# Optimization experiments

Measured on AMD Instinct MI355X. Metric: run time of the kernel, lower is better.

Reference implementation:

```python
import jax, jax.numpy as jnp
import numpy as np

N = 50000
E = 800000
IN_CH = 256
OUT_CH = 64   # per-head channels (PyG out_channels)
HEADS = 4
NEG_SLOPE = 0.2


def setup_inputs() -> dict:
    key = jax.random.key(0)
    k = jax.random.split(key, 8)
    x = jax.random.normal(k[0], (N, IN_CH), dtype=jnp.float32)
    edge_index = jax.random.randint(k[1], (2, E), 0, N, dtype=jnp.int64)
    # GATConv parameters
    W = jax.random.normal(k[2], (IN_CH, HEADS * OUT_CH), dtype=jnp.float32) * (1.0 / np.sqrt(IN_CH))
    att_src = jax.random.normal(k[3], (HEADS, OUT_CH), dtype=jnp.float32) * 0.1
    att_dst = jax.random.normal(k[4], (HEADS, OUT_CH), dtype=jnp.float32) * 0.1
    bias = jnp.zeros((OUT_CH,), dtype=jnp.float32)
    # residual linear (bias=False)
    W_res = jax.random.normal(k[5], (IN_CH, OUT_CH), dtype=jnp.float32) * (1.0 / np.sqrt(IN_CH))
    return {"x": x, "edge_index": edge_index, "W": W, "att_src": att_src,
            "att_dst": att_dst, "bias": bias, "W_res": W_res}


def _gat_forward(x, edge_index, W, att_src, att_dst, bias, W_res):
    # residual branch
    x_res = x @ W_res                                   # [N, OUT_CH]

    # node transform: [N, H, C]
    xw = (x @ W).reshape(N, HEADS, OUT_CH)
    # per-node attention logits, [N, H]
    a_src = jnp.einsum('nhc,hc->nh', xw, att_src)
    a_dst = jnp.einsum('nhc,hc->nh', xw, att_dst)

    # add self-loops (PyG GATConv default add_self_loops=True)
    loops = jnp.arange(N, dtype=edge_index.dtype)
    src = jnp.concatenate([edge_index[0], loops])       # [E+N]
    dst = jnp.concatenate([edge_index[1], loops])       # [E+N]

    # per-edge logits + leaky relu, [E+N, H]
    alpha = jax.nn.leaky_relu(a_src[src] + a_dst[dst], NEG_SLOPE)

    # segment softmax over destination nodes
    m = jax.ops.segment_max(alpha, dst, num_segments=N)    # [N, H]
    e = jnp.exp(alpha - m[dst])
    denom = jax.ops.segment_sum(e, dst, num_segments=N)    # [N, H]
    a = e / denom[dst]                                     # [E+N, H]
    # (dropout p=0.1 on attention coeffs is identity in eval mode)

    # weighted scatter-aggregate: [N, H, C]
    msgs = xw[src] * a[:, :, None]
    out = jax.ops.segment_sum(msgs, dst, num_segments=N)

    # concat=False -> mean over heads, then bias
    x_conv = out.mean(axis=1) + bias                     # [N, OUT_CH]
    return jax.nn.relu(x_conv + x_res)


def reference(x, edge_index, W, att_src, att_dst, bias, W_res):
    return _gat_forward(x, edge_index, W, att_src, att_dst, bias, W_res)
```

## Files before the change

kernel.cpp:

```cpp
#include <hip/hip_runtime.h>
#include <math.h>

#define N_NODES 50000
#define N_EDGES 800000
#define IN_CH   256
#define OUT_CH  64
#define HEADS   4
#define NEG_SLOPE 0.2f
#define NCOLS   320
#define NTILES  20
#define NKK     8
#define PACK_BLOCKS 40
#define GEMM_BLOCKS 782
#define NBINS   391
#define P1_BLOCKS 256
#define EPB     3125
#define AGG_BLOCKS 6250
#define STASH_CAP 2816

typedef __attribute__((ext_vector_type(8))) short short8;
typedef __attribute__((ext_vector_type(4))) float f32x4;

__device__ __forceinline__ float lrelu(float v) {
    return v > 0.f ? v : NEG_SLOPE * v;
}
__device__ __forceinline__ unsigned bf16_rne(float f) {
    unsigned u = __float_as_uint(f);
    return (u + 0x7FFFu + ((u >> 16) & 1u)) >> 16;
}
__device__ __forceinline__ unsigned pack2(float lo, float hi) {
    return bf16_rne(lo) | (bf16_rne(hi) << 16);
}
__device__ __forceinline__ float bflo(unsigned u) { return __uint_as_float(u << 16); }
__device__ __forceinline__ float bfhi(unsigned u) { return __uint_as_float(u & 0xFFFF0000u); }
__device__ __forceinline__ short8 as_short8(uint4 u) {
    union { uint4 u4; short8 s8; } cv; cv.u4 = u; return cv.s8;
}

__global__ __launch_bounds__(256) void pack_B(
    const float* __restrict__ W, const float* __restrict__ Wres,
    uint4* __restrict__ Bp)
{
    const int idx  = blockIdx.x * 256 + threadIdx.x;
    const int kk   = idx / (NTILES * 64);
    const int rem  = idx - kk * (NTILES * 64);
    const int t    = rem >> 6;
    const int lane = rem & 63;
    const int colL = lane & 15, quad = lane >> 4;
    const int col  = t * 16 + colL;
    const int k0   = kk * 32 + quad * 8;
    float v[8];
    #pragma unroll
    for (int j = 0; j < 8; ++j) {
        const int k = k0 + j;
        v[j] = (col < IN_CH) ? W[(size_t)k * IN_CH + col]
                             : Wres[(size_t)k * OUT_CH + (col - IN_CH)];
    }
    uint4 u;
    u.x = pack2(v[0], v[1]); u.y = pack2(v[2], v[3]);
    u.z = pack2(v[4], v[5]); u.w = pack2(v[6], v[7]);
    Bp[(kk * NTILES + t) * 64 + lane] = u;
}

__global__ __launch_bounds__(256) void gemm_hist(
    const float* __restrict__ x, const uint4* __restrict__ Bp,
    uint2* __restrict__ xw2, float* __restrict__ xres,
    const int* __restrict__ ei, int* __restrict__ M,
    const float* __restrict__ attS, const float* __restrict__ attD,
    float* __restrict__ asrc, float* __restrict__ adst)
{
    __shared__ uint4 Alds[4 * NKK * 64];
    __shared__ float logS[64][HEADS];
    __shared__ float logD[64][HEADS];

    if (blockIdx.x >= GEMM_BLOCKS) {
        const int blk = blockIdx.x - GEMM_BLOCKS;
        int* lh = (int*)Alds;
        for (int b = threadIdx.x; b < NBINS; b += 256) lh[b] = 0;
        __syncthreads();
        const int e0 = blk * EPB;
        #pragma unroll
        for (int r = 0; r < 13; ++r) {
            const int idx = (r << 8) + threadIdx.x;
            if (idx < EPB)
                atomicAdd(&lh[ei[N_EDGES + e0 + idx] >> 7], 1);
        }
        __syncthreads();
        for (int b = threadIdx.x; b < NBINS; b += 256)
            M[(size_t)b * P1_BLOCKS + blk] = lh[b];
        return;
    }

    const int tid = threadIdx.x;
    const int n0  = blockIdx.x * 64;

    logS[tid >> 2][tid & 3] = 0.f;
    logD[tid >> 2][tid & 3] = 0.f;

    #pragma unroll
    for (int i = 0; i < 8; ++i) {
        const int e    = i * 256 + tid;
        const int g    = e >> 9;
        const int kk   = (e >> 6) & 7;
        const int lane = e & 63;
        const int cL   = lane & 15, qd = lane >> 4;
        const int row  = n0 + g * 16 + cL;
        const int k0   = kk * 32 + qd * 8;
        uint4 u = make_uint4(0u, 0u, 0u, 0u);
        if (row < N_NODES) {
            const float4 a = *reinterpret_cast<const float4*>(x + (size_t)row * IN_CH + k0);
            const float4 b = *reinterpret_cast<const float4*>(x + (size_t)row * IN_CH + k0 + 4);
            u.x = pack2(a.x, a.y); u.y = pack2(a.z, a.w);
            u.z = pack2(b.x, b.y); u.w = pack2(b.z, b.w);
        }
        Alds[(g * NKK + kk) * 64 + lane] = u;
    }
    __syncthreads();

    const int lane = tid & 63;
    const int wv   = tid >> 6;
    const int colL = lane & 15, quad = lane >> 4;

    f32x4 acc[4][5];
    #pragma unroll
    for (int rg = 0; rg < 4; ++rg)
        #pragma unroll
        for (int j = 0; j < 5; ++j) acc[rg][j] = (f32x4){0.f, 0.f, 0.f, 0.f};

    for (int kk = 0; kk < NKK; ++kk) {
        uint4 bu[5];
        #pragma unroll
        for (int j = 0; j < 5; ++j)
            bu[j] = Bp[(kk * NTILES + j * 4 + wv) * 64 + lane];
        #pragma unroll
        for (int rg = 0; rg < 4; ++rg) {
            const short8 a = as_short8(Alds[(rg * NKK + kk) * 64 + lane]);
            #pragma unroll
            for (int j = 0; j < 5; ++j)
                acc[rg][j] = __builtin_amdgcn_mfma_f32_16x16x32_bf16(
                    a, as_short8(bu[j]), acc[rg][j], 0, 0, 0);
        }
    }

    #pragma unroll
    for (int rg = 0; rg < 4; ++rg) {
        #pragma unroll
        for (int r = 0; r < 4; ++r) {
            const int row = n0 + rg * 16 + quad * 4 + r;
            if (row < N_NODES) {
                xw2[(size_t)row * 64 + wv * 16 + colL] = make_uint2(
                    pack2(acc[rg][0][r], acc[rg][1][r]),
                    pack2(acc[rg][2][r], acc[rg][3][r]));
                xres[(size_t)row * OUT_CH + wv * 16 + colL] = acc[rg][4][r];
            }
        }
    }

    float aSr[HEADS], aDr[HEADS];
    #pragma unroll
    for (int h = 0; h < HEADS; ++h) {
        aSr[h] = attS[h * 64 + wv * 16 + colL];
        aDr[h] = attD[h * 64 + wv * 16 + colL];
    }
    #pragma unroll
    for (int rg = 0; rg < 4; ++rg) {
        #pragma unroll
        for (int h = 0; h < HEADS; ++h) {
            #pragma unroll
            for (int r = 0; r < 4; ++r) {
                float vS = acc[rg][h][r] * aSr[h];
                float vD = acc[rg][h][r] * aDr[h];
                #pragma unroll
                for (int m = 1; m < 16; m <<= 1) {
                    vS += __shfl_xor(vS, m);
                    vD += __shfl_xor(vD, m);
                }
                if (colL == 0) {
                    atomicAdd(&logS[rg * 16 + quad * 4 + r][h], vS);
                    atomicAdd(&logD[rg * 16 + quad * 4 + r][h], vD);
                }
            }
        }
    }
    __syncthreads();
    {
        const int rl = tid >> 2, h = tid & 3;
        const int row = n0 + rl;
        if (row < N_NODES) {
            asrc[(size_t)row * HEADS + h] = logS[rl][h];
            adst[(size_t)row * HEADS + h] = logD[rl][h];
        }
    }
}

__global__ __launch_bounds__(256) void binscan_M(
    int* __restrict__ M, int* __restrict__ binCnt)
{
    __shared__ int ws[4];
    const int t = threadIdx.x, lane = t & 63, w = t >> 6;
    const int b = blockIdx.x;
    const int v = M[(size_t)b * P1_BLOCKS + t];
    int sc = v;
    #pragma unroll
    for (int off = 1; off < 64; off <<= 1) {
        const int n = __shfl_up(sc, off);
        if (lane >= off) sc += n;
    }
    if (lane == 63) ws[w] = sc;
    __syncthreads();
    int prefix = 0;
    for (int j = 0; j < w; ++j) prefix += ws[j];
    M[(size_t)b * P1_BLOCKS + t] = prefix + sc - v;
    if (t == 255) binCnt[b] = prefix + sc;
}

__global__ __launch_bounds__(256) void part_mid(
    const int* __restrict__ ei, const int* __restrict__ M,
    const int* __restrict__ binCnt, unsigned* __restrict__ mid)
{
    __shared__ int bc[NBINS];
    __shared__ int bs[NBINS];
    __shared__ int baseL[NBINS];
    __shared__ int lh[NBINS];
    __shared__ int ws[4];
    const int t = threadIdx.x, lane = t & 63, wv = t >> 6;
    const int blk = blockIdx.x;

    for (int b = t; b < NBINS; b += 256) {
        bc[b] = binCnt[b];
        baseL[b] = M[(size_t)b * P1_BLOCKS + blk];
        lh[b] = 0;
    }
    __syncthreads();

    int tot0;
    {
        const int v = bc[t];
        int sc = v;
        #pragma unroll
        for (int off = 1; off < 64; off <<= 1) {
            const int n = __shfl_up(sc, off);
            if (lane >= off) sc += n;
        }
        if (lane == 63) ws[wv] = sc;
        __syncthreads();
        int prefix = 0;
        for (int j = 0; j < wv; ++j) prefix += ws[j];
        bs[t] = prefix + sc - v;
        tot0 = ws[0] + ws[1] + ws[2] + ws[3];
        __syncthreads();
    }
    {
        const int i2 = 256 + t;
        const int v = (i2 < NBINS) ? bc[i2] : 0;
        int sc = v;
        #pragma unroll
        for (int off = 1; off < 64; off <<= 1) {
            const int n = __shfl_up(sc, off);
            if (lane >= off) sc += n;
        }
        if (lane == 63) ws[wv] = sc;
        __syncthreads();
        int prefix = 0;
        for (int j = 0; j < wv; ++j) prefix += ws[j];
        if (i2 < NBINS) bs[i2] = tot0 + prefix + sc - v;
        __syncthreads();
    }
    for (int b = t; b < NBINS; b += 256) baseL[b] += bs[b];
    __syncthreads();

    const int e0 = blk * EPB;
    #pragma unroll
    for (int r = 0; r < 13; ++r) {
        const int idx = (r << 8) + t;
        if (idx < EPB) {
            const int e = e0 + idx;
            const int d = ei[N_EDGES + e];
            const int b = d >> 7;
            const int pos = atomicAdd(&lh[b], 1);
            mid[baseL[b] + pos] = ((unsigned)(d & 127) << 17) | (unsigned)ei[e];
        }
    }
}

__global__ __launch_bounds__(256) void scatter_fine2(
    const unsigned* __restrict__ mid, const int* __restrict__ binCnt,
    int* __restrict__ cnt, int* __restrict__ lscan, int* __restrict__ esrc)
{
    __shared__ int ws[4];
    __shared__ int c128[128];
    __shared__ int o128[128];
    __shared__ int w0tot;
    __shared__ unsigned stash[STASH_CAP];
    const int t = threadIdx.x, lane = t & 63, wv = t >> 6;
    const int b = blockIdx.x;

    int acc = 0;
    for (int j = t; j < NBINS; j += 256)
        if (j < b) acc += binCnt[j];
    #pragma unroll
    for (int off = 32; off >= 1; off >>= 1) acc += __shfl_xor(acc, off);
    if (lane == 0) ws[wv] = acc;
    if (t < 128) c128[t] = 0;
    __syncthreads();
    const int base = ws[0] + ws[1] + ws[2] + ws[3];
    const int n = binCnt[b];

    for (int i = t; i < n; i += 256) {
        const unsigned m = mid[base + i];
        if (i < STASH_CAP) stash[i] = m;
        atomicAdd(&c128[m >> 17], 1);
    }
    __syncthreads();

    if (t < 128) {
        const int v = c128[t];
        int sc = v;
        #pragma unroll
        for (int off = 1; off < 64; off <<= 1) {
            const int nn = __shfl_up(sc, off);
            if (lane >= off) sc += nn;
        }
        if (t == 63) w0tot = sc;
        __syncthreads();
        const int ex = sc - v + (t >= 64 ? w0tot : 0);
        o128[t] = ex;
        const int d = (b << 7) + t;
        if (d < N_NODES) {
            cnt[d] = v;
            lscan[d] = base + ex;
        }
        c128[t] = 0;
    } else {
        __syncthreads();
    }
    __syncthreads();

    for (int i = t; i < n; i += 256) {
        const unsigned m = (i < STASH_CAP) ? stash[i] : mid[base + i];
        const int dlo = (int)(m >> 17);
        const int pos = atomicAdd(&c128[dlo], 1);
        esrc[base + o128[dlo] + pos] = (int)(m & 0x1FFFFu);
    }
}

__global__ __launch_bounds__(256) void aggregate(
    const int* __restrict__ esrc, const int* __restrict__ lscan,
    const int* __restrict__ cnt,
    const float* __restrict__ asrc, const float* __restrict__ adst,
    const uint2* __restrict__ xw2, const float* __restrict__ xres,
    const float* __restrict__ bias, float* __restrict__ out,
    const int d0)
{
    __shared__ float4 wbuf[4][64];
    __shared__ int    sbuf[4][64];
    const int t = threadIdx.x;
    const int lane = t & 63;
    const int wv   = t >> 6;

    const int d = d0 + blockIdx.x * 4 + wv;
    const int row = lscan[d];
    const int deg = cnt[d];
    const float4 ad = *reinterpret_cast<const float4*>(adst + (size_t)d * 4);
    const char* xwB = (const char*)xw2;
    const int laneB = lane << 3;

    float dn0 = 0.f, dn1 = 0.f, dn2 = 0.f, dn3 = 0.f;
    float ac0 = 0.f, ac1 = 0.f, ac2 = 0.f, ac3 = 0.f;

    for (int base = 0; base < deg; base += 64) {
        const int m = min(64, deg - base);
        if (lane < m) {
            const int s = esrc[row + base + lane];
            const float4 as = *reinterpret_cast<const float4*>(asrc + (size_t)s * 4);
            const float e0 = __expf(lrelu(as.x + ad.x));
            const float e1 = __expf(lrelu(as.y + ad.y));
            const float e2 = __expf(lrelu(as.z + ad.z));
            const float e3 = __expf(lrelu(as.w + ad.w));
            dn0 += e0; dn1 += e1; dn2 += e2; dn3 += e3;
            wbuf[wv][lane] = make_float4(e0, e1, e2, e3);
            sbuf[wv][lane] = s << 9;
        }
        int j = 0;
        for (; j + 4 <= m; j += 4) {
            uint2 v0 = *(const uint2*)(xwB + sbuf[wv][j]     + laneB);
            uint2 v1 = *(const uint2*)(xwB + sbuf[wv][j + 1] + laneB);
            uint2 v2 = *(const uint2*)(xwB + sbuf[wv][j + 2] + laneB);
            uint2 v3 = *(const uint2*)(xwB + sbuf[wv][j + 3] + laneB);
            {
                const float4 w = wbuf[wv][j];
                ac0 = fmaf(w.x, bflo(v0.x), ac0); ac1 = fmaf(w.y, bfhi(v0.x), ac1);
                ac2 = fmaf(w.z, bflo(v0.y), ac2); ac3 = fmaf(w.w, bfhi(v0.y), ac3);
            }
            {
                const float4 w = wbuf[wv][j + 1];
                ac0 = fmaf(w.x, bflo(v1.x), ac0); ac1 = fmaf(w.y, bfhi(v1.x), ac1);
                ac2 = fmaf(w.z, bflo(v1.y), ac2); ac3 = fmaf(w.w, bfhi(v1.y), ac3);
            }
            {
                const float4 w = wbuf[wv][j + 2];
                ac0 = fmaf(w.x, bflo(v2.x), ac0); ac1 = fmaf(w.y, bfhi(v2.x), ac1);
                ac2 = fmaf(w.z, bflo(v2.y), ac2); ac3 = fmaf(w.w, bfhi(v2.y), ac3);
            }
            {
                const float4 w = wbuf[wv][j + 3];
                ac0 = fmaf(w.x, bflo(v3.x), ac0); ac1 = fmaf(w.y, bfhi(v3.x), ac1);
                ac2 = fmaf(w.z, bflo(v3.y), ac2); ac3 = fmaf(w.w, bfhi(v3.y), ac3);
            }
        }
        for (; j < m; ++j) {
            const float4 w = wbuf[wv][j];
            const uint2 v = *(const uint2*)(xwB + sbuf[wv][j] + laneB);
            ac0 = fmaf(w.x, bflo(v.x), ac0);
            ac1 = fmaf(w.y, bfhi(v.x), ac1);
            ac2 = fmaf(w.z, bflo(v.y), ac2);
            ac3 = fmaf(w.w, bfhi(v.y), ac3);
        }
    }

    #pragma unroll
    for (int off = 32; off >= 1; off >>= 1) {
        dn0 += __shfl_xor(dn0, off);
        dn1 += __shfl_xor(dn1, off);
        dn2 += __shfl_xor(dn2, off);
        dn3 += __shfl_xor(dn3, off);
    }
    const float4 asd = *reinterpret_cast<const float4*>(asrc + (size_t)d * 4);
    const float s0 = __expf(lrelu(asd.x + ad.x));
    const float s1 = __expf(lrelu(asd.y + ad.y));
    const float s2 = __expf(lrelu(asd.z + ad.z));
    const float s3 = __expf(lrelu(asd.w + ad.w));
    const uint2 u = xw2[(size_t)d * 64 + lane];
    ac0 = fmaf(s0, bflo(u.x), ac0); ac1 = fmaf(s1, bfhi(u.x), ac1);
    ac2 = fmaf(s2, bflo(u.y), ac2); ac3 = fmaf(s3, bfhi(u.y), ac3);
    const float i0 = 0.25f / (dn0 + s0);
    const float i1 = 0.25f / (dn1 + s1);
    const float i2 = 0.25f / (dn2 + s2);
    const float i3 = 0.25f / (dn3 + s3);
    const float v = ac0 * i0 + ac1 * i1 + ac2 * i2 + ac3 * i3
                  + bias[lane] + xres[(size_t)d * OUT_CH + lane];
    out[(size_t)d * OUT_CH + lane] = fmaxf(v, 0.f);
}

extern "C" void kernel_launch(void* const* d_in, const int* in_sizes, int n_in,
                              void* d_out, int out_size, void* d_ws, size_t ws_size,
                              hipStream_t stream) {
    const float* x    = (const float*)d_in[0];
    const int*   ei   = (const int*)d_in[1];
    const float* W    = (const float*)d_in[2];
    const float* attS = (const float*)d_in[3];
    const float* attD = (const float*)d_in[4];
    const float* bias = (const float*)d_in[5];
    const float* Wres = (const float*)d_in[6];
    float* out = (float*)d_out;

    char* p = (char*)d_ws;
    uint4*    Bp      = (uint4*)p;    p += (size_t)NKK * NTILES * 64 * 16;
    uint2*    xw2     = (uint2*)p;    p += (size_t)N_NODES * 64 * 8;
    float*    xres    = (float*)p;    p += (size_t)N_NODES * OUT_CH * 4;
    float*    asrc    = (float*)p;    p += (size_t)N_NODES * HEADS * 4;
    float*    adst    = (float*)p;    p += (size_t)N_NODES * HEADS * 4;
    int*      M       = (int*)p;      p += (size_t)NBINS * P1_BLOCKS * 4;
    int*      binCnt  = (int*)p;      p += 512 * 4;
    int*      cnt     = (int*)p;      p += (size_t)N_NODES * 4;
    int*      lscan   = (int*)p;      p += (size_t)N_NODES * 4;
    unsigned* mid     = (unsigned*)p; p += (size_t)N_EDGES * 4;
    int*      esrc    = (int*)p;      p += (size_t)N_EDGES * 4;

    pack_B<<<PACK_BLOCKS, 256, 0, stream>>>(W, Wres, Bp);
    gemm_hist<<<GEMM_BLOCKS + P1_BLOCKS, 256, 0, stream>>>(
        x, Bp, xw2, xres, ei, M, attS, attD, asrc, adst);
    binscan_M<<<NBINS, 256, 0, stream>>>(M, binCnt);
    part_mid<<<P1_BLOCKS, 256, 0, stream>>>(ei, M, binCnt, mid);
    scatter_fine2<<<NBINS, 256, 0, stream>>>(mid, binCnt, cnt, lscan, esrc);
    aggregate<<<AGG_BLOCKS, 256, 0, stream>>>(
        esrc, lscan, cnt, asrc, adst, xw2, xres, bias, out, 0);
    aggregate<<<AGG_BLOCKS, 256, 0, stream>>>(
        esrc, lscan, cnt, asrc, adst, xw2, xres, bias, out, 25000);
}
```

Baseline: 237.5 us.

## Halve partition bin width, precompute bin starts, and merge aggregate launches

The counting-sort bins shrink from 128 to 64 destination nodes, doubling the bin count. That gives the fine scatter kernel twice as many smaller blocks and lets it drop to a single-wave 64-entry scan. Bin start offsets are now written once by part_mid instead of every scatter block re-summing all previous bin counts. The two half-range aggregate launches are merged into one launch, removing a kernel boundary. The cost is a larger histogram matrix M and a smaller LDS stash, so more large bins fall back to re-reading from global memory.

```diff
diff --git a/kernel.cpp b/kernel.cpp
--- a/kernel.cpp
+++ b/kernel.cpp
@@ -12,11 +12,11 @@
 #define NKK     8
 #define PACK_BLOCKS 40
 #define GEMM_BLOCKS 782
-#define NBINS   391
+#define NBINS   782
 #define P1_BLOCKS 256
 #define EPB     3125
-#define AGG_BLOCKS 6250
-#define STASH_CAP 2816
+#define AGG_BLOCKS 12500
+#define STASH_CAP 1280
 
 typedef __attribute__((ext_vector_type(8))) short short8;
 typedef __attribute__((ext_vector_type(4))) float f32x4;
@@ -83,7 +83,7 @@
         for (int r = 0; r < 13; ++r) {
             const int idx = (r << 8) + threadIdx.x;
             if (idx < EPB)
-                atomicAdd(&lh[ei[N_EDGES + e0 + idx] >> 7], 1);
+                atomicAdd(&lh[ei[N_EDGES + e0 + idx] >> 6], 1);
         }
         __syncthreads();
         for (int b = threadIdx.x; b < NBINS; b += 256)
@@ -216,7 +216,8 @@
 
 __global__ __launch_bounds__(256) void part_mid(
     const int* __restrict__ ei, const int* __restrict__ M,
-    const int* __restrict__ binCnt, unsigned* __restrict__ mid)
+    const int* __restrict__ binCnt, int* __restrict__ binStart,
+    unsigned* __restrict__ mid)
 {
     __shared__ int bc[NBINS];
     __shared__ int bs[NBINS];
@@ -233,40 +234,27 @@
     }
     __syncthreads();
 
-    int tot0;
-    {
-        const int v = bc[t];
+    int carry = 0;
+    for (int c = 0; c < 4; ++c) {
+        const int i = (c << 8) + t;
+        const int v = (i < NBINS) ? bc[i] : 0;
         int sc = v;
         #pragma unroll
-        for (int off = 1; off < 64; off <<= 1) {
-            const int n = __shfl_up(sc, off);
-            if (lane >= off) sc += n;
+        for (int o = 1; o < 64; o <<= 1) {
+            const int n = __shfl_up(sc, o);
+            if (lane >= o) sc += n;
         }
         if (lane == 63) ws[wv] = sc;
         __syncthreads();
         int prefix = 0;
         for (int j = 0; j < wv; ++j) prefix += ws[j];
-        bs[t] = prefix + sc - v;
-        tot0 = ws[0] + ws[1] + ws[2] + ws[3];
+        if (i < NBINS) bs[i] = carry + prefix + sc - v;
+        carry += ws[0] + ws[1] + ws[2] + ws[3];
         __syncthreads();
     }
-    {
-        const int i2 = 256 + t;
-        const int v = (i2 < NBINS) ? bc[i2] : 0;
-        int sc = v;
-        #pragma unroll
-        for (int off = 1; off < 64; off <<= 1) {
-            const int n = __shfl_up(sc, off);
-            if (lane >= off) sc += n;
-        }
-        if (lane == 63) ws[wv] = sc;
-        __syncthreads();
-        int prefix = 0;
-        for (int j = 0; j < wv; ++j) prefix += ws[j];
-        if (i2 < NBINS) bs[i2] = tot0 + prefix + sc - v;
-        __syncthreads();
-    }
     for (int b = t; b < NBINS; b += 256) baseL[b] += bs[b];
+    if (blk == 0)
+        for (int b = t; b < NBINS; b += 256) binStart[b] = bs[b];
     __syncthreads();
 
     const int e0 = blk * EPB;
@@ -276,71 +264,60 @@
         if (idx < EPB) {
             const int e = e0 + idx;
             const int d = ei[N_EDGES + e];
-            const int b = d >> 7;
+            const int b = d >> 6;
             const int pos = atomicAdd(&lh[b], 1);
-            mid[baseL[b] + pos] = ((unsigned)(d & 127) << 17) | (unsigned)ei[e];
+            mid[baseL[b] + pos] = ((unsigned)(d & 63) << 17) | (unsigned)ei[e];
         }
     }
 }
 
 __global__ __launch_bounds__(256) void scatter_fine2(
-    const unsigned* __restrict__ mid, const int* __restrict__ binCnt,
+    const unsigned* __restrict__ mid, const int* __restrict__ binStart,
+    const int* __restrict__ binCnt,
     int* __restrict__ cnt, int* __restrict__ lscan, int* __restrict__ esrc)
 {
-    __shared__ int ws[4];
-    __shared__ int c128[128];
-    __shared__ int o128[128];
-    __shared__ int w0tot;
+    __shared__ int c64[64];
+    __shared__ int o64[64];
     __shared__ unsigned stash[STASH_CAP];
-    const int t = threadIdx.x, lane = t & 63, wv = t >> 6;
+    const int t = threadIdx.x;
     const int b = blockIdx.x;
 
-    int acc = 0;
-    for (int j = t; j < NBINS; j += 256)
-        if (j < b) acc += binCnt[j];
-    #pragma unroll
-    for (int off = 32; off >= 1; off >>= 1) acc += __shfl_xor(acc, off);
-    if (lane == 0) ws[wv] = acc;
-    if (t < 128) c128[t] = 0;
-    __syncthreads();
-    const int base = ws[0] + ws[1] + ws[2] + ws[3];
+    const int base = binStart[b];
     const int n = binCnt[b];
+    if (t < 64) c64[t] = 0;
+    __syncthreads();
 
     for (int i = t; i < n; i += 256) {
         const unsigned m = mid[base + i];
         if (i < STASH_CAP) stash[i] = m;
-        atomicAdd(&c128[m >> 17], 1);
-    }
-    __syncthreads();
-
-    if (t < 128) {
-        const int v = c128[t];
+        atomicAdd(&c64[m >> 17], 1);
+    }
+    __syncthreads();
+
+    if (t < 64) {
+        const int v = c64[t];
         int sc = v;
         #pragma unroll
-        for (int off = 1; off < 64; off <<= 1) {
-            const int nn = __shfl_up(sc, off);
-            if (lane >= off) sc += nn;
-        }
-        if (t == 63) w0tot = sc;
-        __syncthreads();
-        const int ex = sc - v + (t >= 64 ? w0tot : 0);
-        o128[t] = ex;
-        const int d = (b << 7) + t;
+        for (int o = 1; o < 64; o <<= 1) {
+            const int nn = __shfl_up(sc, o);
+            if (t >= o) sc += nn;
+        }
+        const int ex = sc - v;
+        o64[t] = ex;
+        const int d = (b << 6) + t;
         if (d < N_NODES) {
             cnt[d] = v;
             lscan[d] = base + ex;
         }
-        c128[t] = 0;
-    } else {
-        __syncthreads();
+        c64[t] = 0;
     }
     __syncthreads();
 
     for (int i = t; i < n; i += 256) {
         const unsigned m = (i < STASH_CAP) ? stash[i] : mid[base + i];
         const int dlo = (int)(m >> 17);
-        const int pos = atomicAdd(&c128[dlo], 1);
-        esrc[base + o128[dlo] + pos] = (int)(m & 0x1FFFFu);
+        const int pos = atomicAdd(&c64[dlo], 1);
+        esrc[base + o64[dlo] + pos] = (int)(m & 0x1FFFFu);
     }
 }
 
@@ -349,8 +326,7 @@
     const int* __restrict__ cnt,
     const float* __restrict__ asrc, const float* __restrict__ adst,
     const uint2* __restrict__ xw2, const float* __restrict__ xres,
-    const float* __restrict__ bias, float* __restrict__ out,
-    const int d0)
+    const float* __restrict__ bias, float* __restrict__ out)
 {
     __shared__ float4 wbuf[4][64];
     __shared__ int    sbuf[4][64];
@@ -358,7 +334,7 @@
     const int lane = t & 63;
     const int wv   = t >> 6;
 
-    const int d = d0 + blockIdx.x * 4 + wv;
+    const int d = blockIdx.x * 4 + wv;
     const int row = lscan[d];
     const int deg = cnt[d];
     const float4 ad = *reinterpret_cast<const float4*>(adst + (size_t)d * 4);
@@ -461,7 +437,8 @@
     float*    asrc    = (float*)p;    p += (size_t)N_NODES * HEADS * 4;
     float*    adst    = (float*)p;    p += (size_t)N_NODES * HEADS * 4;
     int*      M       = (int*)p;      p += (size_t)NBINS * P1_BLOCKS * 4;
-    int*      binCnt  = (int*)p;      p += 512 * 4;
+    int*      binCnt  = (int*)p;      p += 1024 * 4;
+    int*      binStart= (int*)p;      p += 1024 * 4;
     int*      cnt     = (int*)p;      p += (size_t)N_NODES * 4;
     int*      lscan   = (int*)p;      p += (size_t)N_NODES * 4;
     unsigned* mid     = (unsigned*)p; p += (size_t)N_EDGES * 4;
@@ -471,10 +448,9 @@
     gemm_hist<<<GEMM_BLOCKS + P1_BLOCKS, 256, 0, stream>>>(
         x, Bp, xw2, xres, ei, M, attS, attD, asrc, adst);
     binscan_M<<<NBINS, 256, 0, stream>>>(M, binCnt);
-    part_mid<<<P1_BLOCKS, 256, 0, stream>>>(ei, M, binCnt, mid);
-    scatter_fine2<<<NBINS, 256, 0, stream>>>(mid, binCnt, cnt, lscan, esrc);
+    part_mid<<<P1_BLOCKS, 256, 0, stream>>>(ei, M, binCnt, binStart, mid);
+    scatter_fine2<<<NBINS, 256, 0, stream>>>(
+        mid, binStart, binCnt, cnt, lscan, esrc);
     aggregate<<<AGG_BLOCKS, 256, 0, stream>>>(
-        esrc, lscan, cnt, asrc, adst, xw2, xres, bias, out, 0);
-    aggregate<<<AGG_BLOCKS, 256, 0, stream>>>(
-        esrc, lscan, cnt, asrc, adst, xw2, xres, bias, out, 25000);
-}
+        esrc, lscan, cnt, asrc, adst, xw2, xres, bias, out);
+}
```

New measurement: 229.5 us. 1.03x faster.
